# Kernel optimization log

Hardware: AMD Instinct MI355X
Metric: run time of the kernel (lower is better)

## Reference

```python
import jax, jax.numpy as jnp
import numpy as np

B, T, V = 128, 128, 30000
DE, DP, PV = 300, 30, 50
H = 300
HEADS = 6
LA, LL = 5, 24
POL = 3
RED = 10
NEG = -1e9


def entmax15(x):
    # exact 1.5-entmax along last axis (sorting algorithm, Peters & Martins 2019)
    d = x.shape[-1]
    x = x / 2.0
    x = x - jnp.max(x, axis=-1, keepdims=True)
    xs = -jnp.sort(-x, axis=-1)                      # descending
    rho = jnp.arange(1, d + 1, dtype=x.dtype)
    mean = jnp.cumsum(xs, axis=-1) / rho
    meansq = jnp.cumsum(xs * xs, axis=-1) / rho
    ss = rho * (meansq - mean * mean)
    delta = (1.0 - ss) / rho
    tau = mean - jnp.sqrt(jnp.maximum(delta, 0.0))
    support = jnp.sum((tau <= xs).astype(jnp.int32), axis=-1, keepdims=True)
    tau_star = jnp.take_along_axis(tau, support - 1, axis=-1)
    return jnp.square(jnp.maximum(x - tau_star, 0.0))


def lstm_dir(x, mask, Wih, Whh, bih, bhh, reverse):
    # packed-sequence-equivalent LSTM: state frozen / output zeroed at padded steps
    b = x.shape[0]
    h0 = jnp.zeros((b, Whh.shape[1]), x.dtype)

    def step(carry, inp):
        h, c = carry
        xt, mt = inp
        g = xt @ Wih.T + h @ Whh.T + (bih + bhh)
        i, f, gg, o = jnp.split(g, 4, axis=-1)       # torch gate order i,f,g,o
        c_new = jax.nn.sigmoid(f) * c + jax.nn.sigmoid(i) * jnp.tanh(gg)
        h_new = jax.nn.sigmoid(o) * jnp.tanh(c_new)
        m = mt[:, None]
        return (jnp.where(m, h_new, h), jnp.where(m, c_new, c)), jnp.where(m, h_new, 0.0)

    _, outs = jax.lax.scan(step, (h0, h0),
                           (jnp.swapaxes(x, 0, 1), jnp.swapaxes(mask, 0, 1)),
                           reverse=reverse)
    return jnp.swapaxes(outs, 0, 1)


def se_layer(x, valid, w1, b1, w2, b2):
    # SELayer over the SEQUENCE dim (channel == max_len); x: [b,t,d], valid: [b,t]
    y = jnp.mean(x, axis=-1)                         # adaptive avg-pool over (1, d)
    y = jax.nn.relu(y @ w1.T + b1) @ w2.T + b2
    y = y + jnp.where(valid > 0, 0.0, NEG)           # mask_2
    y = jax.nn.softmax(y, axis=1)
    return x * y[..., None]


def gcn(x, A, W, b):
    # D @ A @ D @ x @ W + b with D = diag((rowsum(A)+1)^-0.5)
    dn = (jnp.sum(A, axis=2) + 1.0) ** -0.5
    An = dn[:, :, None] * A * dn[:, None, :]
    return jnp.einsum('bij,bjd->bid', An, x) @ W + b


def _forward(text_indices, aspect_indices, left_indices, pos_indices, asp_post, height,
             adj, embed_matrix, pos_emb_w, Wih_f, Whh_f, bih_f, bhh_f,
             Wih_b, Whh_b, bih_b, bhh_b, wq, bq, wk, bk,
             se_w1, se_b1, se_w2, se_b2, gc1_w, gc1_b, gc2_w, gc2_b,
             affine1, affine2, fc_w, fc_b):
    b, t = text_indices.shape
    nonpad = text_indices != 0
    valid = nonpad.astype(jnp.float32)               # mask_ squeezed -> [b,t]
    text_len = jnp.sum(nonpad, axis=-1)
    aspect_real_len = jnp.sum(aspect_indices != 0, axis=-1)
    left_len = jnp.sum(left_indices != 0, axis=-1)   # aspect_double_idx = [left_len,left_len]

    # embedding; overwrite aspect position with mean aspect embedding
    text = embed_matrix[text_indices]
    am = (aspect_indices != 0).astype(jnp.float32)[..., None]
    asp_mean = jnp.sum(embed_matrix[aspect_indices] * am, axis=1) / aspect_real_len[:, None].astype(jnp.float32)
    text = text.at[jnp.arange(b), asp_post].set(asp_mean)
    embs = jnp.concatenate([text, pos_emb_w[pos_indices]], axis=-1)

    lenmask = jnp.arange(t)[None, :] < text_len[:, None]
    text_out = jnp.concatenate([
        lstm_dir(embs, lenmask, Wih_f, Whh_f, bih_f, bhh_f, False),
        lstm_dir(embs, lenmask, Wih_b, Whh_b, bih_b, bhh_b, True)], axis=-1)  # [b,t,2H]

    # multi-head entmax attention -> semantic adjacency
    dk = (2 * H) // HEADS
    q = (text_out @ wq.T + bq).reshape(b, t, HEADS, dk).transpose(0, 2, 1, 3)
    k = (text_out @ wk.T + bk).reshape(b, t, HEADS, dk).transpose(0, 2, 1, 3)
    scores = jnp.einsum('bhqd,bhkd->bhqk', q, k) / (dk ** 0.5)
    scores = jnp.where(nonpad[:, None, None, :], scores, NEG)
    adj_sem = jnp.mean(entmax15(scores), axis=1)     # average over heads
    eye = jnp.eye(t, dtype=adj_sem.dtype)
    adj_sem = adj_sem * (1.0 - eye) + eye            # zero diagonal, add identity
    adj_sem = valid[:, :, None] * adj_sem

    se = lambda z: se_layer(z, valid, se_w1, se_b1, se_w2, se_b2)
    # (the first x = relu(gc1(..,adj)); x = relu(gc2(..,adj)) branch is dead code:
    #  x is overwritten before use, so only the x_sem path matters)
    x_sem = jax.nn.relu(gcn(se(text_out), adj_sem, gc1_w, gc1_b))
    x = jax.nn.relu(gcn(se(x_sem), adj, gc2_w, gc2_b))

    A1 = jax.nn.softmax(jnp.einsum('bid,bjd->bij', x @ affine1, x_sem), axis=-1)
    A2 = jax.nn.softmax(jnp.einsum('bid,bjd->bij', x_sem @ affine2, x), axis=-1)
    out = jnp.concatenate([jnp.einsum('bij,bjd->bid', A1, x_sem),
                           jnp.einsum('bij,bjd->bid', A2, x)], axis=-1)  # [b,t,4H]
    aspmask = (jnp.arange(t)[None, :] == left_len[:, None]).astype(jnp.float32)
    pooled = jnp.sum(out * aspmask[..., None], axis=1)  # keep aspect token only
    return pooled @ fc_w + fc_b                         # [b, POL]


def setup_inputs():
    key = jax.random.key(0)
    ks = jax.random.split(key, 36)
    f32 = jnp.float32
    pos_t = jnp.arange(T)[None, :]
    text_len = jax.random.randint(ks[0], (B,), T // 2, T + 1)
    text_indices = jax.random.randint(ks[1], (B, T), 1, V) * (pos_t < text_len[:, None])
    asp_len = jax.random.randint(ks[2], (B,), 1, LA + 1)
    aspect_indices = jax.random.randint(ks[3], (B, LA), 1, V) * (jnp.arange(LA)[None, :] < asp_len[:, None])
    left_len = jax.random.randint(ks[4], (B,), 1, LL + 1)
    left_indices = jax.random.randint(ks[5], (B, LL), 1, V) * (jnp.arange(LL)[None, :] < left_len[:, None])
    pos_indices = jax.random.randint(ks[6], (B, T), 1, PV) * (pos_t < text_len[:, None])
    vmask = (pos_t < text_len[:, None]).astype(f32)
    adj = (jax.random.uniform(ks[7], (B, T, T)) < 0.08).astype(f32)
    adj = adj * vmask[:, :, None] * vmask[:, None, :]
    asp_post = left_len                              # aspect sits right after left context
    height = jax.random.randint(ks[8], (B, T + 1), 1, 12)

    def rn(k, shape, scale=0.05):
        return jax.random.normal(k, shape, dtype=f32) * scale

    params = dict(
        embed_matrix=rn(ks[9], (V, DE), 0.5),
        pos_emb_w=rn(ks[10], (PV, DP), 0.5).at[0].set(0.0),
        Wih_f=rn(ks[11], (4 * H, DE + DP)), Whh_f=rn(ks[12], (4 * H, H)),
        bih_f=rn(ks[13], (4 * H,)), bhh_f=rn(ks[14], (4 * H,)),
        Wih_b=rn(ks[15], (4 * H, DE + DP)), Whh_b=rn(ks[16], (4 * H, H)),
        bih_b=rn(ks[17], (4 * H,)), bhh_b=rn(ks[18], (4 * H,)),
        wq=rn(ks[19], (2 * H, 2 * H)), bq=rn(ks[20], (2 * H,)),
        wk=rn(ks[21], (2 * H, 2 * H)), bk=rn(ks[22], (2 * H,)),
        se_w1=rn(ks[23], (T // RED, T)), se_b1=rn(ks[24], (T // RED,)),
        se_w2=rn(ks[25], (T, T // RED)), se_b2=rn(ks[26], (T,)),
        gc1_w=rn(ks[27], (2 * H, 2 * H)), gc1_b=rn(ks[28], (2 * H,)),
        gc2_w=rn(ks[29], (2 * H, 2 * H)), gc2_b=rn(ks[30], (2 * H,)),
        affine1=rn(ks[31], (2 * H, 2 * H)), affine2=rn(ks[32], (2 * H, 2 * H)),
        fc_w=rn(ks[33], (4 * H, POL)), fc_b=rn(ks[34], (POL,)),
    )
    return dict(text_indices=text_indices, aspect_indices=aspect_indices,
                left_indices=left_indices, pos_indices=pos_indices,
                asp_post=asp_post, height=height, adj=adj, **params)


def reference(text_indices, aspect_indices, left_indices, pos_indices, asp_post, height,
              adj, embed_matrix, pos_emb_w, Wih_f, Whh_f, bih_f, bhh_f,
              Wih_b, Whh_b, bih_b, bhh_b, wq, bq, wk, bk,
              se_w1, se_b1, se_w2, se_b2, gc1_w, gc1_b, gc2_w, gc2_b,
              affine1, affine2, fc_w, fc_b):
    return _forward(text_indices, aspect_indices, left_indices, pos_indices, asp_post, height,
                    adj, embed_matrix, pos_emb_w, Wih_f, Whh_f, bih_f, bhh_f,
                    Wih_b, Whh_b, bih_b, bhh_b, wq, bq, wk, bk,
                    se_w1, se_b1, se_w2, se_b2, gc1_w, gc1_b, gc2_w, gc2_b,
                    affine1, affine2, fc_w, fc_b)
```

## Files before the change

kernel.cpp:

```cpp
#include <hip/hip_runtime.h>

typedef unsigned short ushort_t;
typedef unsigned int   uint_t;
typedef __attribute__((ext_vector_type(8))) short short8;
typedef __attribute__((ext_vector_type(4))) float floatx4;

#define NEGV -1000000000.0f

__device__ __forceinline__ float bf2f(ushort_t h){ return __uint_as_float(((uint_t)h)<<16); }
__device__ __forceinline__ ushort_t f2bf(float f){
  uint_t u = __float_as_uint(f);
  uint_t r = u + 0x7fffu + ((u>>16)&1u);
  return (ushort_t)(r>>16);
}
__device__ __forceinline__ float wredsum(float v){ for(int o=32;o;o>>=1) v += __shfl_xor(v,o); return v; }
__device__ __forceinline__ float wredmax(float v){ for(int o=32;o;o>>=1) v = fmaxf(v,__shfl_xor(v,o)); return v; }
__device__ __forceinline__ int   wredsumi(int v){ for(int o=32;o;o>>=1) v += __shfl_xor(v,o); return v; }

__device__ __forceinline__ short8 ldg_cohr(const ushort_t* p){
  short8 r;
  asm volatile("global_load_dwordx4 %0, %1, off sc0 sc1"
               : "=&v"(r) : "v"(p) : "memory");
  return r;
}
__device__ __forceinline__ void stg_b128_cohr(ushort_t* p, short8 v){
  asm volatile("global_store_dwordx4 %0, %1, off sc0 sc1" :: "v"(p), "v"(v) : "memory");
}

__device__ __forceinline__ float fsig(float x){ return 1.f/(1.f+__expf(-x)); }
__device__ __forceinline__ float ftanh(float x){ return 1.f - 2.f/(1.f+__expf(2.f*x)); }

__global__ void k_cvt8(const void* __restrict__ src, ushort_t* __restrict__ dst,
                       long n, const ushort_t* __restrict__ probe_src){
  __shared__ int sflag;
  if (threadIdx.x < 64){
    ushort_t u = probe_src[2*threadIdx.x];
    int e = (u>>7)&0xFF;
    int c = (e>=100 && e<=140) ? 1 : 0;
    c = wredsumi(c);
    if (threadIdx.x==0) sflag = (c>32) ? 1 : 0;
  }
  __syncthreads();
  bool isbf = (sflag!=0);
  long base = (blockIdx.x*256L + threadIdx.x)*8;
  if (base>=n) return;
  if (isbf){
    if (base+8<=n) *(uint4*)(dst+base) = *(const uint4*)((const ushort_t*)src+base);
    else for (long i=base;i<n;i++) dst[i]=((const ushort_t*)src)[i];
  } else {
    const float* s = (const float*)src;
    if (base+8<=n){
      float4 v0 = *(const float4*)(s+base);
      float4 v1 = *(const float4*)(s+base+4);
      ushort_t o[8] = {f2bf(v0.x),f2bf(v0.y),f2bf(v0.z),f2bf(v0.w),
                       f2bf(v1.x),f2bf(v1.y),f2bf(v1.z),f2bf(v1.w)};
      *(uint4*)(dst+base) = *(uint4*)o;
    } else {
      for (long i=base;i<n;i++) dst[i]=f2bf(s[i]);
    }
  }
}

struct CvtTab { const void* src[25]; ushort_t* dst[25]; long n[25]; };

__global__ void k_cvt8_multi(CvtTab tab, const ushort_t* __restrict__ probe_src){
  __shared__ int sflag;
  if (threadIdx.x < 64){
    ushort_t u = probe_src[2*threadIdx.x];
    int e = (u>>7)&0xFF;
    int c = (e>=100 && e<=140) ? 1 : 0;
    c = wredsumi(c);
    if (threadIdx.x==0) sflag = (c>32) ? 1 : 0;
  }
  __syncthreads();
  bool isbf = (sflag!=0);
  int ix = blockIdx.y;
  long n = tab.n[ix];
  long base = (blockIdx.x*256L + threadIdx.x)*8;
  if (base>=n) return;
  const void* src = tab.src[ix];
  ushort_t* dst = tab.dst[ix];
  if (isbf){
    if (base+8<=n) *(uint4*)(dst+base) = *(const uint4*)((const ushort_t*)src+base);
    else for (long i=base;i<n;i++) dst[i]=((const ushort_t*)src)[i];
  } else {
    const float* s = (const float*)src;
    if (base+8<=n){
      float4 v0 = *(const float4*)(s+base);
      float4 v1 = *(const float4*)(s+base+4);
      ushort_t o[8] = {f2bf(v0.x),f2bf(v0.y),f2bf(v0.z),f2bf(v0.w),
                       f2bf(v1.x),f2bf(v1.y),f2bf(v1.z),f2bf(v1.w)};
      *(uint4*)(dst+base) = *(uint4*)o;
    } else {
      for (long i=base;i<n;i++) dst[i]=f2bf(s[i]);
    }
  }
}

__device__ __forceinline__ bool probe_is_bf16(const ushort_t* probe_src){
  int c=0;
  #pragma unroll 1
  for (int i=0;i<64;i++){
    ushort_t u = probe_src[2*i];
    int e = (u>>7)&0xFF;
    c += (e>=100 && e<=140) ? 1 : 0;
  }
  return c>32;
}

__global__ void k_lens(const int* __restrict__ ti, const int* __restrict__ li,
                       int* __restrict__ nonpad, int* __restrict__ text_len,
                       int* __restrict__ left_len){
  int b = blockIdx.x, t = threadIdx.x;
  nonpad[b*128+t] = (ti[b*128+t]!=0) ? 1 : 0;
  if (t==0){
    int c=0; for (int k2=0;k2<128;k2++) c += (ti[b*128+k2]!=0);
    text_len[b]=c;
    int l=0; for (int k2=0;k2<24;k2++) l += (li[b*24+k2]!=0);
    left_len[b]=l;
  }
}

__global__ void k_aspmean(const int* __restrict__ ai, const ushort_t* __restrict__ em,
                          float* __restrict__ asp_mean){
  int b = blockIdx.x;
  int idxs[5]; int cnt=0;
  for (int a=0;a<5;a++){ int ix=ai[b*5+a]; idxs[a]=ix; cnt += (ix!=0); }
  float inv = 1.0f/(float)cnt;
  for (int d=threadIdx.x; d<300; d+=128){
    float s=0.f;
    for (int a=0;a<5;a++) if (idxs[a]) s += bf2f(em[(long)idxs[a]*300+d]);
    asp_mean[b*300+d] = s*inv;
  }
}

__global__ void k_embs(const int* __restrict__ ti, const int* __restrict__ pi,
                       const int* __restrict__ asp_post,
                       const ushort_t* __restrict__ em, const ushort_t* __restrict__ pe,
                       const float* __restrict__ asp_mean, ushort_t* __restrict__ embs){
  int blk = blockIdx.x;
  int b = blk>>7, t = blk&127;
  int ap = asp_post[b];
  int tix = ti[b*128+t];
  int pix = pi[b*128+t];
  for (int col=threadIdx.x; col<336; col+=128){
    ushort_t v;
    if (col<300) v = (t==ap) ? f2bf(asp_mean[b*300+col]) : em[(long)tix*300+col];
    else if (col<330) v = pe[pix*30 + (col-300)];
    else v = 0;
    embs[(long)(b*128+t)*336 + col] = v;
  }
}

__global__ void k_padwih2(const ushort_t* __restrict__ src, ushort_t* __restrict__ dst){
  int i = blockIdx.x*blockDim.x + threadIdx.x;
  if (i >= 1280*336) return;
  int r = i/336, k = i - r*336;
  int j = r>>2, gate = r&3;
  ushort_t v = 0;
  if (j<300 && k<330) v = src[(long)(gate*300+j)*330 + k];
  dst[i] = v;
}

__global__ void k_padwhh2(const ushort_t* __restrict__ src, ushort_t* __restrict__ dst){
  int i = blockIdx.x*blockDim.x + threadIdx.x;
  if (i >= 1280*320) return;
  int r = i/320, k = i - r*320;
  int j = r>>2, gate = r&3;
  ushort_t v = 0;
  if (j<300 && k<300) v = src[(long)(gate*300+j)*300 + k];
  dst[i] = v;
}

__global__ void k_biassum2(const ushort_t* __restrict__ a, const ushort_t* __restrict__ b,
                           float* __restrict__ dst){
  int i = blockIdx.x*blockDim.x + threadIdx.x;
  if (i>=1280) return;
  int j = i>>2, g = i&3;
  dst[i] = (j<300) ? (bf2f(a[g*300+j]) + bf2f(b[g*300+j])) : 0.f;
}

__global__ void k_biascvt(const ushort_t* __restrict__ a, float* __restrict__ dst, int n){
  int i = blockIdx.x*blockDim.x + threadIdx.x;
  if (i<n) dst[i] = bf2f(a[i]);
}

__global__ void k_padzero(ushort_t* __restrict__ qh, ushort_t* __restrict__ kh){
  int i = blockIdx.x*blockDim.x + threadIdx.x;
  if (i >= 98304*4*2) return;
  int half = (i >= 98304*4) ? 1 : 0;
  int j = i - half*98304*4;
  int row = j>>2, c = 100 + (j&3);
  (half ? kh : qh)[(long)row*104 + c] = 0;
}

template<int TB, int MODE>
__global__ __launch_bounds__(256) void gemm_k(
    int M, int N, int K,
    const ushort_t* __restrict__ A, long lda, long sAz,
    const ushort_t* __restrict__ B, long ldb, long sBz,
    float* __restrict__ Cf, ushort_t* __restrict__ Cb, long ldc, long sCz,
    const float* __restrict__ bias, int relu,
    const float* __restrict__ rowscale,
    const int* __restrict__ nonpad)
{
  __shared__ ushort_t As[128*40];
  __shared__ ushort_t Bs[128*40];
  const int tid = threadIdx.x;
  const int m0 = blockIdx.x*128, n0 = blockIdx.y*128;
  const int z = blockIdx.z;
  const ushort_t* Ap = A + (long)z*sAz;
  const ushort_t* Bp = B + (long)z*sBz;
  floatx4 acc[4][4];
  #pragma unroll
  for (int i=0;i<4;i++)
    #pragma unroll
    for (int j=0;j<4;j++){ acc[i][j][0]=0.f; acc[i][j][1]=0.f; acc[i][j][2]=0.f; acc[i][j][3]=0.f; }
  const int w = tid>>6, wm = w&1, wn = w>>1;
  const int lane = tid&63, lr = lane&15, lq = lane>>4;

  for (int k0=0;k0<K;k0+=32){
    #pragma unroll
    for (int c2=0;c2<2;c2++){
      int ch = tid + 256*c2;
      int row = ch>>2, kc = (ch&3)*8;
      int gr = m0+row, gk = k0+kc;
      uint4 v{};
      if (gr<M && gk<K) v = *(const uint4*)(Ap + (long)gr*lda + gk);
      *(uint4*)(&As[row*40+kc]) = v;
    }
    if (TB){
      #pragma unroll
      for (int c2=0;c2<2;c2++){
        int ch = tid + 256*c2;
        int row = ch>>2, kc = (ch&3)*8;
        int gn = n0+row, gk = k0+kc;
        uint4 v{};
        if (gn<N && gk<K) v = *(const uint4*)(Bp + (long)gn*ldb + gk);
        int sw = kc ^ (((row>>3)&3)<<3);
        *(uint4*)(&Bs[row*40+sw]) = v;
      }
    } else {
      #pragma unroll
      for (int c2=0;c2<2;c2++){
        int ch = tid + 256*c2;
        int kk = ch>>4, nc = (ch&15)*8;
        int gk = k0+kk, gn = n0+nc;
        uint4 v{};
        if (gk<K && gn<N) v = *(const uint4*)(Bp + (long)gk*ldb + gn);
        uint_t wsv[4] = {v.x, v.y, v.z, v.w};
        #pragma unroll
        for (int e=0;e<8;e++){
          ushort_t hv = (e&1) ? (ushort_t)(wsv[e>>1]>>16) : (ushort_t)(wsv[e>>1]&0xffffu);
          int n = nc+e;
          int sw = kk ^ (((n>>3)&3)<<3);
          Bs[n*40+sw] = hv;
        }
      }
    }
    __syncthreads();
    short8 af[4], bfv[4];
    #pragma unroll
    for (int i=0;i<4;i++) af[i] = *(const short8*)(&As[(wm*64+i*16+lr)*40 + lq*8]);
    #pragma unroll
    for (int j=0;j<4;j++){
      int n = wn*64+j*16+lr;
      int sw = (lq*8) ^ (((n>>3)&3)<<3);
      bfv[j] = *(const short8*)(&Bs[n*40+sw]);
    }
    #pragma unroll
    for (int i=0;i<4;i++)
      #pragma unroll
      for (int j=0;j<4;j++)
        acc[i][j] = __builtin_amdgcn_mfma_f32_16x16x32_bf16(af[i], bfv[j], acc[i][j], 0,0,0);
    __syncthreads();
  }

  #pragma unroll
  for (int i=0;i<4;i++){
    #pragma unroll
    for (int j=0;j<4;j++){
      #pragma unroll
      for (int r=0;r<4;r++){
        int row = m0 + wm*64 + i*16 + lq*4 + r;
        int col = n0 + wn*64 + j*16 + lr;
        if (row<M && col<N){
          float v = acc[i][j][r];
          if (rowscale) v *= rowscale[(long)z*M + row];
          if (bias) v += bias[col];
          if (relu && v<0.f) v = 0.f;
          if (MODE==1){
            Cb[(long)z*sCz + (long)row*ldc + col] = f2bf(v);
          } else if (MODE==2){
            int b = row>>7, t = row&127;
            int h = col/100, d = col - h*100;
            Cb[ ((long)((b*6+h)*128+t))*104 + d ] = f2bf(v);
          } else if (MODE==3){
            v *= 0.1f;
            if (!nonpad[(z/6)*128 + col]) v = NEGV;
            Cf[(long)z*sCz + (long)row*ldc + col] = v;
          }
        }
      }
    }
  }
}

#define BLD 328
#define HXD 40

__global__ __launch_bounds__(512,1) void lstm2_k(
    const ushort_t* __restrict__ whh2f, const ushort_t* __restrict__ whh2b,
    const ushort_t* __restrict__ gipf, const ushort_t* __restrict__ gipb,
    ushort_t* __restrict__ hbuf,
    int* __restrict__ barr,
    ushort_t* __restrict__ text_out, const int* __restrict__ text_len,
    ushort_t* __restrict__ dumpb)
{
  __shared__ ushort_t Blds[64*BLD];
  __shared__ ushort_t hx[64*HXD];

  const int bx = blockIdx.x;
  const int slice = bx % 10;
  const int grp   = bx / 10;
  const int dir = grp & 1, bh = grp >> 1;
  const ushort_t* __restrict__ whh = dir ? whh2b : whh2f;
  const ushort_t* __restrict__ gip = dir ? gipb : gipf;
  ushort_t* hb = hbuf + (long)dir * (2L*128*320);
  int* flg = barr + grp*160;

  const int tid = threadIdx.x;
  const int w = tid>>6, lane = tid&63, lr = lane&15, lq = lane>>4;
  const int wm = w&3, wn = w>>2;

  short8 a[2][10];
  #pragma unroll
  for (int mi=0;mi<2;mi++){
    const ushort_t* ar = whh + (long)(slice*128 + (wm*2+mi)*16 + lr)*320 + lq*8;
    #pragma unroll
    for (int kf=0;kf<10;kf++) a[mi][kf] = *(const short8*)(ar + kf*32);
  }
  #pragma unroll
  for (int mi=0;mi<2;mi++)
    #pragma unroll
    for (int kf=0;kf<10;kf++)
      asm volatile("" : "+v"(a[mi][kf]));

  int jj_[2], b_[2], bl_[2], tl_[2];
  #pragma unroll
  for (int mi=0;mi<2;mi++) jj_[mi] = slice*32 + wm*8 + mi*4 + lq;
  #pragma unroll
  for (int ni=0;ni<2;ni++){
    bl_[ni] = wn*32 + ni*16 + lr;
    b_[ni]  = bh*64 + bl_[ni];
    tl_[ni] = text_len[b_[ni]];
  }

  const int boff0 = (wn*32+   lr)*BLD + lq*8;
  const int boff1 = (wn*32+16+lr)*BLD + lq*8;

  float    c_st[2][2];
  ushort_t h_st[2][2];
  #pragma unroll
  for (int mi=0;mi<2;mi++){ c_st[mi][0]=0.f; c_st[mi][1]=0.f; h_st[mi][0]=0; h_st[mi][1]=0; }

  uint2 gp[2][2];
  {
    int t0 = dir ? 127 : 0;
    #pragma unroll
    for (int mi=0;mi<2;mi++)
      #pragma unroll
      for (int ni=0;ni<2;ni++)
        gp[mi][ni] = *(const uint2*)(gip + ((long)(b_[ni]*128 + t0))*1280 + jj_[mi]*4);
  }

  for (int s=0; s<128; s++){
    const int t = dir ? (127-s) : s;
    const ushort_t* rb = hb + (long)(s&1)*(128L*320);
    ushort_t*       wb = hb + (long)((s+1)&1)*(128L*320);

    short8 tmp[5]; int ro_[5], ch_[5];
    #pragma unroll
    for (int k=0;k<5;k++){
      int c = tid + k*512;
      int row = c/40, ch = c - row*40;
      ro_[k]=row; ch_[k]=ch;
      tmp[k] = ldg_cohr(rb + (long)(bh*64+row)*320 + ch*8);
    }
    asm volatile("s_waitcnt vmcnt(0)" ::: "memory");
    __builtin_amdgcn_sched_barrier(0);
    #pragma unroll
    for (int k=0;k<5;k++)
      *(short8*)(&Blds[ro_[k]*BLD + ch_[k]*8]) = tmp[k];
    __syncthreads();

    floatx4 acc[2][2];
    #pragma unroll
    for (int mi=0;mi<2;mi++)
      #pragma unroll
      for (int ni=0;ni<2;ni++){ acc[mi][ni][0]=0.f; acc[mi][ni][1]=0.f; acc[mi][ni][2]=0.f; acc[mi][ni][3]=0.f; }
    #pragma unroll
    for (int kf=0;kf<10;kf++){
      short8 b0 = *(const short8*)(&Blds[boff0 + kf*32]);
      short8 b1 = *(const short8*)(&Blds[boff1 + kf*32]);
      acc[0][0] = __builtin_amdgcn_mfma_f32_16x16x32_bf16(a[0][kf], b0, acc[0][0], 0,0,0);
      acc[0][1] = __builtin_amdgcn_mfma_f32_16x16x32_bf16(a[0][kf], b1, acc[0][1], 0,0,0);
      acc[1][0] = __builtin_amdgcn_mfma_f32_16x16x32_bf16(a[1][kf], b0, acc[1][0], 0,0,0);
      acc[1][1] = __builtin_amdgcn_mfma_f32_16x16x32_bf16(a[1][kf], b1, acc[1][1], 0,0,0);
    }

    ushort_t tov[2][2];
    #pragma unroll
    for (int mi=0;mi<2;mi++){
      #pragma unroll
      for (int ni=0;ni<2;ni++){
        float g_i = acc[mi][ni][0] + bf2f((ushort_t)(gp[mi][ni].x & 0xffffu));
        float g_f = acc[mi][ni][1] + bf2f((ushort_t)(gp[mi][ni].x >> 16));
        float g_g = acc[mi][ni][2] + bf2f((ushort_t)(gp[mi][ni].y & 0xffffu));
        float g_o = acc[mi][ni][3] + bf2f((ushort_t)(gp[mi][ni].y >> 16));
        float ig = fsig(g_i);
        float fg = fsig(g_f);
        float gg = ftanh(g_g);
        float og = fsig(g_o);
        float cn = fg*c_st[mi][ni] + ig*gg;
        float hn = og*ftanh(cn);
        bool m = (t < tl_[ni]);
        if (m) c_st[mi][ni] = cn;
        ushort_t hv = m ? f2bf(hn) : h_st[mi][ni];
        h_st[mi][ni] = hv;
        hx[bl_[ni]*HXD + wm*8 + mi*4 + lq] = hv;
        tov[mi][ni] = m ? f2bf(hn) : (ushort_t)0;
      }
    }
    __syncthreads();

    if (tid < 256){
      int row = tid>>2, jj8 = (tid&3)*8;
      short8 hvv = *(const short8*)(&hx[row*HXD + jj8]);
      stg_b128_cohr(wb + (long)(bh*64+row)*320 + slice*32 + jj8, hvv);
    }
    #pragma unroll
    for (int mi=0;mi<2;mi++)
      #pragma unroll
      for (int ni=0;ni<2;ni++){
        ushort_t* toa = (jj_[mi] < 300)
          ? &text_out[((long)(b_[ni]*128 + t))*600 + dir*300 + jj_[mi]]
          : &dumpb[tid*4 + mi*2 + ni];
        *toa = tov[mi][ni];
      }
    {
      int tn = dir ? ((s<127) ? (126-s) : 127) : ((s<127) ? (s+1) : 0);
      #pragma unroll
      for (int mi=0;mi<2;mi++)
        #pragma unroll
        for (int ni=0;ni<2;ni++)
          gp[mi][ni] = *(const uint2*)(gip + ((long)(b_[ni]*128 + tn))*1280 + jj_[mi]*4);
    }
    asm volatile("s_waitcnt vmcnt(8)" ::: "memory");
    __syncthreads();

    if (tid==0)
      __hip_atomic_store(&flg[slice*16], s+1, __ATOMIC_RELAXED, __HIP_MEMORY_SCOPE_AGENT);
    {
      bool done = false;
      do {
        int f = 0x7fffffff;
        if (lane < 10)
          f = __hip_atomic_load(&flg[lane*16], __ATOMIC_RELAXED, __HIP_MEMORY_SCOPE_AGENT);
        done = (bool)__all(f >= s+1);
        if (!done) __builtin_amdgcn_s_sleep(1);
      } while(!done);
    }
  }
}

__global__ __launch_bounds__(64) void k_entmax(float* __restrict__ p){
  long row = blockIdx.x;
  float* base = p + row*128;
  __shared__ float xo[128], xs[128], c1[128], c2[128];
  int t = threadIdx.x;
  float a = base[t]*0.5f, b = base[t+64]*0.5f;
  float m = wredmax(fmaxf(a,b));
  a -= m; b -= m;
  xo[t]=a; xo[t+64]=b; xs[t]=a; xs[t+64]=b;
  __syncthreads();
  for (int k2=2;k2<=128;k2<<=1){
    for (int j=k2>>1;j>0;j>>=1){
      int i = ((t & ~(j-1))<<1) | (t & (j-1));
      int ixj = i | j;
      float vi = xs[i], vj = xs[ixj];
      bool blk = (i & k2)==0;
      bool sw = blk ? (vi < vj) : (vi > vj);
      __syncthreads();
      if (sw){ xs[i]=vj; xs[ixj]=vi; }
      __syncthreads();
    }
  }
  c1[t]=xs[t];       c2[t]=xs[t]*xs[t];
  c1[t+64]=xs[t+64]; c2[t+64]=xs[t+64]*xs[t+64];
  __syncthreads();
  for (int d=1; d<128; d<<=1){
    float a1 = (t>=d)     ? c1[t-d]    : 0.f;
    float a2 = (t>=d)     ? c2[t-d]    : 0.f;
    float b1 = (t+64>=d)  ? c1[t+64-d] : 0.f;
    float b2 = (t+64>=d)  ? c2[t+64-d] : 0.f;
    float x1=c1[t], y1=c2[t], x2=c1[t+64], y2=c2[t+64];
    __syncthreads();
    c1[t]=x1+a1; c2[t]=y1+a2; c1[t+64]=x2+b1; c2[t+64]=y2+b2;
    __syncthreads();
  }
  float tau_a, tau_b; int cnt=0;
  {
    float rho = (float)(t+1);
    float mean = c1[t]/rho, msq = c2[t]/rho;
    float ss = rho*(msq-mean*mean);
    float delta = (1.f-ss)/rho;
    tau_a = mean - sqrtf(fmaxf(delta,0.f));
    cnt += (tau_a <= xs[t]) ? 1 : 0;
  }
  {
    float rho = (float)(t+65);
    float mean = c1[t+64]/rho, msq = c2[t+64]/rho;
    float ss = rho*(msq-mean*mean);
    float delta = (1.f-ss)/rho;
    tau_b = mean - sqrtf(fmaxf(delta,0.f));
    cnt += (tau_b <= xs[t+64]) ? 1 : 0;
  }
  __syncthreads();
  c1[t]=tau_a; c1[t+64]=tau_b;
  __syncthreads();
  int support = wredsumi(cnt);
  support = (support<1) ? 1 : ((support>128) ? 128 : support);
  float tau_star = c1[support-1];
  float oa = fmaxf(xo[t]-tau_star, 0.f);
  float ob = fmaxf(xo[t+64]-tau_star, 0.f);
  base[t] = oa*oa; base[t+64] = ob*ob;
}

__global__ void k_adjsem(const float* __restrict__ p, const int* __restrict__ nonpad,
                         ushort_t* __restrict__ adj_sem){
  int idx = blockIdx.x*blockDim.x + threadIdx.x;
  if (idx >= 128*128*128) return;
  int b = idx>>14, rem = idx&16383, i = rem>>7, j = rem&127;
  float s = 0.f;
  for (int h=0;h<6;h++) s += p[(long)b*98304 + h*16384 + i*128 + j];
  float v = s/6.0f;
  if (i==j) v = 1.0f;
  if (!nonpad[b*128+i]) v = 0.f;
  adj_sem[idx] = f2bf(v);
}

__global__ __launch_bounds__(64) void k_dn(const ushort_t* __restrict__ src, float* __restrict__ dnv){
  long row = blockIdx.x;
  int l = threadIdx.x;
  float s = bf2f(src[row*128+l]) + bf2f(src[row*128+l+64]);
  s = wredsum(s);
  if (l==0) dnv[row] = 1.0f/sqrtf(s+1.0f);
}

__global__ __launch_bounds__(64) void k_mean(const ushort_t* __restrict__ X, float* __restrict__ ymean){
  long row = blockIdx.x;
  float s=0.f;
  for (int d=threadIdx.x; d<600; d+=64) s += bf2f(X[row*600+d]);
  s = wredsum(s);
  if (threadIdx.x==0) ymean[row] = s/600.0f;
}

__global__ void k_senet(const float* __restrict__ ymean,
                        const ushort_t* __restrict__ w1, const ushort_t* __restrict__ b1,
                        const ushort_t* __restrict__ w2, const ushort_t* __restrict__ b2,
                        const int* __restrict__ nonpad, float* __restrict__ ysoft){
  int b = blockIdx.x, t = threadIdx.x;
  __shared__ float yv[128], z1[12], red[128];
  yv[t] = ymean[b*128+t];
  __syncthreads();
  if (t<12){
    float s = bf2f(b1[t]);
    for (int k2=0;k2<128;k2++) s += yv[k2]*bf2f(w1[t*128+k2]);
    z1[t] = fmaxf(s,0.f);
  }
  __syncthreads();
  float v = bf2f(b2[t]);
  for (int r=0;r<12;r++) v += z1[r]*bf2f(w2[t*12+r]);
  if (!nonpad[b*128+t]) v += NEGV;
  red[t]=v; __syncthreads();
  for (int s2=64;s2>0;s2>>=1){ if (t<s2) red[t]=fmaxf(red[t],red[t+s2]); __syncthreads(); }
  float mx = red[0]; __syncthreads();
  float e = expf(v-mx);
  red[t]=e; __syncthreads();
  for (int s2=64;s2>0;s2>>=1){ if (t<s2) red[t]+=red[t+s2]; __syncthreads(); }
  float sm = red[0];
  ysoft[b*128+t] = e/sm;
}

__global__ void k_scale2(const ushort_t* __restrict__ X, const float* __restrict__ ysoft,
                         const float* __restrict__ dnv, ushort_t* __restrict__ out){
  int i = blockIdx.x*blockDim.x + threadIdx.x;
  if (i >= 128*128*600) return;
  int row = i/600;
  out[i] = f2bf(bf2f(X[i])*ysoft[row]*dnv[row]);
}

__global__ void k_gather(const ushort_t* __restrict__ X, const int* __restrict__ left_len,
                         ushort_t* __restrict__ dst){
  int b = blockIdx.x;
  int lb = left_len[b];
  for (int d=threadIdx.x; d<600; d+=128)
    dst[b*600+d] = X[(long)(b*128+lb)*600+d];
}

__global__ __launch_bounds__(256) void k_pool(const ushort_t* __restrict__ g,
                                              const ushort_t* __restrict__ X,
                                              float* __restrict__ pooled, int poff){
  int b = blockIdx.x, tid = threadIdx.x;
  __shared__ float gs[600], sbuf[128], red[256];
  for (int d=tid; d<600; d+=256) gs[d] = bf2f(g[b*600+d]);
  __syncthreads();
  int wv = tid>>6, lane = tid&63;
  for (int jj=wv; jj<128; jj+=4){
    float s=0.f;
    for (int d=lane; d<600; d+=64) s += gs[d]*bf2f(X[(long)(b*128+jj)*600+d]);
    s = wredsum(s);
    if (lane==0) sbuf[jj]=s;
  }
  __syncthreads();
  float v = (tid<128) ? sbuf[tid] : -3.4e38f;
  red[tid]=v; __syncthreads();
  for (int s2=128;s2>0;s2>>=1){ if (tid<s2) red[tid]=fmaxf(red[tid],red[tid+s2]); __syncthreads(); }
  float mx = red[0]; __syncthreads();
  float e = (tid<128) ? expf(v-mx) : 0.f;
  red[tid]=e; __syncthreads();
  for (int s2=128;s2>0;s2>>=1){ if (tid<s2) red[tid]+=red[tid+s2]; __syncthreads(); }
  float sm = red[0]; __syncthreads();
  if (tid<128) sbuf[tid] = e/sm;
  __syncthreads();
  for (int d=tid; d<600; d+=256){
    float acc=0.f;
    for (int j=0;j<128;j++) acc += sbuf[j]*bf2f(X[(long)(b*128+j)*600+d]);
    pooled[(long)b*1200 + poff + d] = acc;
  }
}

__global__ __launch_bounds__(64) void k_final(const float* __restrict__ pooled,
                                              const ushort_t* __restrict__ fcw,
                                              const ushort_t* __restrict__ fcb,
                                              void* __restrict__ out,
                                              const ushort_t* __restrict__ probe_src){
  bool isbf = probe_is_bf16(probe_src);
  int b = blockIdx.x, lane = threadIdx.x;
  for (int p=0;p<3;p++){
    float s=0.f;
    for (int d=lane; d<1200; d+=64) s += pooled[(long)b*1200+d]*bf2f(fcw[d*3+p]);
    s = wredsum(s);
    if (lane==0){
      float r = s + bf2f(fcb[p]);
      if (isbf) ((ushort_t*)out)[b*3+p] = f2bf(r);
      else      ((float*)out)[b*3+p] = r;
    }
  }
}

extern "C" void kernel_launch(void* const* d_in, const int* in_sizes, int n_in,
                              void* d_out, int out_size, void* d_ws, size_t ws_size,
                              hipStream_t stream) {
  const int*      ti   = (const int*)d_in[0];
  const int*      ai   = (const int*)d_in[1];
  const int*      li   = (const int*)d_in[2];
  const int*      pi   = (const int*)d_in[3];
  const int*      aps  = (const int*)d_in[4];
  const ushort_t* probe = (const ushort_t*)d_in[7];

  char* w = (char*)d_ws; size_t off = 0;
  auto alloc = [&](size_t bytes)->char*{ char* p = w+off; off = (off+bytes+255)&~(size_t)255; return p; };

  int*   text_len = (int*)alloc(512);
  int*   left_len = (int*)alloc(512);
  int*   nonpad   = (int*)alloc(65536);
  float* asp_mean = (float*)alloc(153600);
  float* dn1      = (float*)alloc(65536);
  float* dn2      = (float*)alloc(65536);
  float* ymean    = (float*)alloc(65536);
  float* ysoft    = (float*)alloc(65536);
  ushort_t* wihpf = (ushort_t*)alloc(860160);
  ushort_t* wihpb = (ushort_t*)alloc(860160);
  ushort_t* whh2f = (ushort_t*)alloc(819200);
  ushort_t* whh2b = (ushort_t*)alloc(819200);
  ushort_t* hbuf  = (ushort_t*)alloc(327680);
  int*      barr  = (int*)alloc(4096);
  ushort_t* dumpb = (ushort_t*)alloc(4096);
  float* biasgf   = (float*)alloc(5120);
  float* biasgb   = (float*)alloc(5120);
  float* bqf      = (float*)alloc(2400);
  float* bkf      = (float*)alloc(2400);
  float* gc1bf    = (float*)alloc(2400);
  float* gc2bf    = (float*)alloc(2400);
  ushort_t* g1    = (ushort_t*)alloc(153600);
  ushort_t* g2    = (ushort_t*)alloc(153600);
  ushort_t* xr    = (ushort_t*)alloc(153600);
  ushort_t* xsr   = (ushort_t*)alloc(153600);
  float* pooled   = (float*)alloc(614400);
  ushort_t* adj_c  = (ushort_t*)alloc(4194304);
  ushort_t* pe_c   = (ushort_t*)alloc(2048);
  ushort_t* wihf_c = (ushort_t*)alloc(792000);
  ushort_t* wihb_c = (ushort_t*)alloc(792000);
  ushort_t* whhf_c = (ushort_t*)alloc(720000);
  ushort_t* whhb_c = (ushort_t*)alloc(720000);
  ushort_t* bihf_c = (ushort_t*)alloc(2400);
  ushort_t* bhhf_c = (ushort_t*)alloc(2400);
  ushort_t* bihb_c = (ushort_t*)alloc(2400);
  ushort_t* bhhb_c = (ushort_t*)alloc(2400);
  ushort_t* wq_c   = (ushort_t*)alloc(720000);
  ushort_t* bq_c   = (ushort_t*)alloc(1200);
  ushort_t* wk_c   = (ushort_t*)alloc(720000);
  ushort_t* bk_c   = (ushort_t*)alloc(1200);
  ushort_t* sw1_c  = (ushort_t*)alloc(3072);
  ushort_t* sb1_c  = (ushort_t*)alloc(256);
  ushort_t* sw2_c  = (ushort_t*)alloc(3072);
  ushort_t* sb2_c  = (ushort_t*)alloc(256);
  ushort_t* g1w_c  = (ushort_t*)alloc(720000);
  ushort_t* g1b_c  = (ushort_t*)alloc(1200);
  ushort_t* g2w_c  = (ushort_t*)alloc(720000);
  ushort_t* g2b_c  = (ushort_t*)alloc(1200);
  ushort_t* af1_c  = (ushort_t*)alloc(720000);
  ushort_t* af2_c  = (ushort_t*)alloc(720000);
  ushort_t* fcw_c  = (ushort_t*)alloc(7200);
  ushort_t* fcb_c  = (ushort_t*)alloc(256);
  ushort_t* embs  = (ushort_t*)alloc(11010048);
  ushort_t* textout = (ushort_t*)alloc(19660800);
  char* R = alloc(95420416);
  ushort_t* em_c    = (ushort_t*)(R);
  ushort_t* gip_f   = (ushort_t*)(R);
  ushort_t* gip_b   = (ushort_t*)(R+41943040);
  ushort_t* qh      = (ushort_t*)(R);
  ushort_t* kh      = (ushort_t*)(R+20447232);
  float*    scores  = (float*)(R+40894464);
  ushort_t* adj_sem = (ushort_t*)(R+91226112);
  ushort_t* se_x    = (ushort_t*)(R+40894464);
  ushort_t* Zb      = (ushort_t*)(R+60555264);
  ushort_t* x_sem   = (ushort_t*)(R);
  ushort_t* xb      = (ushort_t*)(R+20447232);
  (void)ws_size; (void)n_in; (void)in_sizes; (void)out_size;

  k_cvt8<<<(9000000/8+255)/256,256,0,stream>>>(d_in[7], em_c, 9000000L, probe);
  k_cvt8<<<(2097152/8+255)/256,256,0,stream>>>(d_in[6], adj_c, 2097152L, probe);
  {
    CvtTab tab;
    const int idx[25] = {8,9,13,10,14,11,12,15,16,17,18,19,20,21,22,23,24,25,26,27,28,29,30,31,32};
    ushort_t* dl[25] = {pe_c,wihf_c,wihb_c,whhf_c,whhb_c,bihf_c,bhhf_c,bihb_c,bhhb_c,
                        wq_c,bq_c,wk_c,bk_c,sw1_c,sb1_c,sw2_c,sb2_c,
                        g1w_c,g1b_c,g2w_c,g2b_c,af1_c,af2_c,fcw_c,fcb_c};
    const long nl[25] = {900,396000,396000,360000,360000,1200,1200,1200,1200,
                         360000,600,360000,600,1536,12,1536,128,
                         360000,600,360000,600,360000,360000,3600,3};
    for (int i=0;i<25;i++){ tab.src[i]=d_in[idx[i]]; tab.dst[i]=dl[i]; tab.n[i]=nl[i]; }
    k_cvt8_multi<<<dim3(194,25),256,0,stream>>>(tab, probe);
  }

  k_lens<<<128,128,0,stream>>>(ti, li, nonpad, text_len, left_len);
  k_aspmean<<<128,128,0,stream>>>(ai, em_c, asp_mean);
  k_embs<<<16384,128,0,stream>>>(ti, pi, aps, em_c, pe_c, asp_mean, embs);
  k_padwih2<<<(1280*336+255)/256,256,0,stream>>>(wihf_c, wihpf);
  k_padwih2<<<(1280*336+255)/256,256,0,stream>>>(wihb_c, wihpb);
  k_padwhh2<<<(1280*320+255)/256,256,0,stream>>>(whhf_c, whh2f);
  k_padwhh2<<<(1280*320+255)/256,256,0,stream>>>(whhb_c, whh2b);
  k_biassum2<<<(1280+255)/256,256,0,stream>>>(bihf_c, bhhf_c, biasgf);
  k_biassum2<<<(1280+255)/256,256,0,stream>>>(bihb_c, bhhb_c, biasgb);
  k_biascvt<<<3,256,0,stream>>>(bq_c, bqf, 600);
  k_biascvt<<<3,256,0,stream>>>(bk_c, bkf, 600);
  k_biascvt<<<3,256,0,stream>>>(g1b_c, gc1bf, 600);
  k_biascvt<<<3,256,0,stream>>>(g2b_c, gc2bf, 600);

  gemm_k<1,1><<<dim3(128,10,1),256,0,stream>>>(16384,1280,336, embs,336,0, wihpf,336,0,
        nullptr, gip_f,1280,0, biasgf,0,nullptr,nullptr);
  gemm_k<1,1><<<dim3(128,10,1),256,0,stream>>>(16384,1280,336, embs,336,0, wihpb,336,0,
        nullptr, gip_b,1280,0, biasgb,0,nullptr,nullptr);

  hipMemsetAsync(hbuf, 0, 327680, stream);
  hipMemsetAsync(barr, 0, 4096, stream);
  lstm2_k<<<40,512,0,stream>>>(whh2f, whh2b, gip_f, gip_b, hbuf, barr, textout, text_len, dumpb);

  k_padzero<<<(98304*4*2+255)/256,256,0,stream>>>(qh, kh);
  gemm_k<1,2><<<dim3(128,5,1),256,0,stream>>>(16384,600,600, textout,600,0, wq_c,600,0,
        nullptr, qh,0,0, bqf,0,nullptr,nullptr);
  gemm_k<1,2><<<dim3(128,5,1),256,0,stream>>>(16384,600,600, textout,600,0, wk_c,600,0,
        nullptr, kh,0,0, bkf,0,nullptr,nullptr);

  gemm_k<1,3><<<dim3(1,1,768),256,0,stream>>>(128,128,104, qh,104,13312, kh,104,13312,
        scores, nullptr, 128, 16384, nullptr,0,nullptr, nonpad);

  k_entmax<<<98304,64,0,stream>>>(scores);

  k_adjsem<<<(2097152+255)/256,256,0,stream>>>(scores, nonpad, adj_sem);
  k_dn<<<16384,64,0,stream>>>(adj_sem, dn1);
  k_dn<<<16384,64,0,stream>>>(adj_c, dn2);

  k_mean<<<16384,64,0,stream>>>(textout, ymean);
  k_senet<<<128,128,0,stream>>>(ymean, sw1_c,sb1_c,sw2_c,sb2_c, nonpad, ysoft);
  k_scale2<<<(9830400+255)/256,256,0,stream>>>(textout, ysoft, dn1, se_x);
  gemm_k<0,1><<<dim3(1,5,128),256,0,stream>>>(128,600,128, adj_sem,128,16384, se_x,600,76800,
        nullptr, Zb,600,76800, nullptr,0, dn1, nullptr);
  gemm_k<0,1><<<dim3(128,5,1),256,0,stream>>>(16384,600,600, Zb,600,0, g1w_c,600,0,
        nullptr, x_sem,600,0, gc1bf,1,nullptr,nullptr);

  k_mean<<<16384,64,0,stream>>>(x_sem, ymean);
  k_senet<<<128,128,0,stream>>>(ymean, sw1_c,sb1_c,sw2_c,sb2_c, nonpad, ysoft);
  k_scale2<<<(9830400+255)/256,256,0,stream>>>(x_sem, ysoft, dn2, se_x);
  gemm_k<0,1><<<dim3(1,5,128),256,0,stream>>>(128,600,128, adj_c,128,16384, se_x,600,76800,
        nullptr, Zb,600,76800, nullptr,0, dn2, nullptr);
  gemm_k<0,1><<<dim3(128,5,1),256,0,stream>>>(16384,600,600, Zb,600,0, g2w_c,600,0,
        nullptr, xb,600,0, gc2bf,1,nullptr,nullptr);

  k_gather<<<128,128,0,stream>>>(xb, left_len, xr);
  k_gather<<<128,128,0,stream>>>(x_sem, left_len, xsr);
  gemm_k<0,1><<<dim3(1,5,1),256,0,stream>>>(128,600,600, xr,600,0, af1_c,600,0,
        nullptr, g1,600,0, nullptr,0,nullptr,nullptr);
  gemm_k<0,1><<<dim3(1,5,1),256,0,stream>>>(128,600,600, xsr,600,0, af2_c,600,0,
        nullptr, g2,600,0, nullptr,0,nullptr,nullptr);
  k_pool<<<128,256,0,stream>>>(g1, x_sem, pooled, 0);
  k_pool<<<128,256,0,stream>>>(g2, xb, pooled, 600);

  k_final<<<128,64,0,stream>>>(pooled, fcw_c, fcb_c, d_out, probe);
}
```

Measured before the change: 1.793 ms.

## Replace cross-block barrier LSTM with per-block batch-group LSTM using LDS hidden state

The recurrent LSTM kernel no longer splits the hidden dimension across 10 cooperating blocks that sync through global-memory flags and coherent global h buffers. Instead each of 16 blocks (1024 threads) owns 16 sequences of one direction, keeps h double-buffered in LDS, and uses only __syncthreads per step. This removes the grid-wide spin barrier and global h round trips. In exchange only 16 CUs are used, and W_hh is re-streamed from global/L2 every step instead of staying in registers, with a non-unrolled k loop.

```diff
diff --git a/kernel.cpp b/kernel.cpp
--- a/kernel.cpp
+++ b/kernel.cpp
@@ -16,16 +16,6 @@
 __device__ __forceinline__ float wredsum(float v){ for(int o=32;o;o>>=1) v += __shfl_xor(v,o); return v; }
 __device__ __forceinline__ float wredmax(float v){ for(int o=32;o;o>>=1) v = fmaxf(v,__shfl_xor(v,o)); return v; }
 __device__ __forceinline__ int   wredsumi(int v){ for(int o=32;o;o>>=1) v += __shfl_xor(v,o); return v; }
-
-__device__ __forceinline__ short8 ldg_cohr(const ushort_t* p){
-  short8 r;
-  asm volatile("global_load_dwordx4 %0, %1, off sc0 sc1"
-               : "=&v"(r) : "v"(p) : "memory");
-  return r;
-}
-__device__ __forceinline__ void stg_b128_cohr(ushort_t* p, short8 v){
-  asm volatile("global_store_dwordx4 %0, %1, off sc0 sc1" :: "v"(p), "v"(v) : "memory");
-}
 
 __device__ __forceinline__ float fsig(float x){ return 1.f/(1.f+__expf(-x)); }
 __device__ __forceinline__ float ftanh(float x){ return 1.f - 2.f/(1.f+__expf(2.f*x)); }
@@ -306,171 +296,96 @@
   }
 }
 
-#define BLD 328
-#define HXD 40
-
-__global__ __launch_bounds__(512,1) void lstm2_k(
+#define HLD 328
+
+__global__ __launch_bounds__(1024,1) void lstm3_k(
     const ushort_t* __restrict__ whh2f, const ushort_t* __restrict__ whh2b,
     const ushort_t* __restrict__ gipf, const ushort_t* __restrict__ gipb,
-    ushort_t* __restrict__ hbuf,
-    int* __restrict__ barr,
-    ushort_t* __restrict__ text_out, const int* __restrict__ text_len,
-    ushort_t* __restrict__ dumpb)
+    ushort_t* __restrict__ text_out, const int* __restrict__ text_len)
 {
-  __shared__ ushort_t Blds[64*BLD];
-  __shared__ ushort_t hx[64*HXD];
+  __shared__ ushort_t hbufs[2][16*HLD];
 
   const int bx = blockIdx.x;
-  const int slice = bx % 10;
-  const int grp   = bx / 10;
-  const int dir = grp & 1, bh = grp >> 1;
+  const int dir = bx & 1, bg = bx >> 1;
   const ushort_t* __restrict__ whh = dir ? whh2b : whh2f;
   const ushort_t* __restrict__ gip = dir ? gipb : gipf;
-  ushort_t* hb = hbuf + (long)dir * (2L*128*320);
-  int* flg = barr + grp*160;
 
   const int tid = threadIdx.x;
   const int w = tid>>6, lane = tid&63, lr = lane&15, lq = lane>>4;
-  const int wm = w&3, wn = w>>2;
-
-  short8 a[2][10];
+
+  for (int i=tid; i<2*16*HLD; i+=1024) ((ushort_t*)hbufs)[i] = 0;
+
+  int jj_[5];
   #pragma unroll
-  for (int mi=0;mi<2;mi++){
-    const ushort_t* ar = whh + (long)(slice*128 + (wm*2+mi)*16 + lr)*320 + lq*8;
-    #pragma unroll
-    for (int kf=0;kf<10;kf++) a[mi][kf] = *(const short8*)(ar + kf*32);
-  }
+  for (int mi=0;mi<5;mi++) jj_[mi] = w*20 + mi*4 + lq;
+  const int b  = bg*16 + lr;
+  const int tl = text_len[b];
+  const long gibase = (long)b*128;
+
+  float    c_st[5];
+  ushort_t h_st[5];
   #pragma unroll
-  for (int mi=0;mi<2;mi++)
-    #pragma unroll
-    for (int kf=0;kf<10;kf++)
-      asm volatile("" : "+v"(a[mi][kf]));
-
-  int jj_[2], b_[2], bl_[2], tl_[2];
-  #pragma unroll
-  for (int mi=0;mi<2;mi++) jj_[mi] = slice*32 + wm*8 + mi*4 + lq;
-  #pragma unroll
-  for (int ni=0;ni<2;ni++){
-    bl_[ni] = wn*32 + ni*16 + lr;
-    b_[ni]  = bh*64 + bl_[ni];
-    tl_[ni] = text_len[b_[ni]];
-  }
-
-  const int boff0 = (wn*32+   lr)*BLD + lq*8;
-  const int boff1 = (wn*32+16+lr)*BLD + lq*8;
-
-  float    c_st[2][2];
-  ushort_t h_st[2][2];
-  #pragma unroll
-  for (int mi=0;mi<2;mi++){ c_st[mi][0]=0.f; c_st[mi][1]=0.f; h_st[mi][0]=0; h_st[mi][1]=0; }
-
-  uint2 gp[2][2];
-  {
-    int t0 = dir ? 127 : 0;
-    #pragma unroll
-    for (int mi=0;mi<2;mi++)
-      #pragma unroll
-      for (int ni=0;ni<2;ni++)
-        gp[mi][ni] = *(const uint2*)(gip + ((long)(b_[ni]*128 + t0))*1280 + jj_[mi]*4);
-  }
-
+  for (int mi=0;mi<5;mi++){ c_st[mi]=0.f; h_st[mi]=0; }
+
+  const ushort_t* abase = whh + (long)(w*80 + lr)*320 + lq*8;
+
+  __syncthreads();
+
+  #pragma unroll 1
   for (int s=0; s<128; s++){
     const int t = dir ? (127-s) : s;
-    const ushort_t* rb = hb + (long)(s&1)*(128L*320);
-    ushort_t*       wb = hb + (long)((s+1)&1)*(128L*320);
-
-    short8 tmp[5]; int ro_[5], ch_[5];
-    #pragma unroll
-    for (int k=0;k<5;k++){
-      int c = tid + k*512;
-      int row = c/40, ch = c - row*40;
-      ro_[k]=row; ch_[k]=ch;
-      tmp[k] = ldg_cohr(rb + (long)(bh*64+row)*320 + ch*8);
-    }
-    asm volatile("s_waitcnt vmcnt(0)" ::: "memory");
-    __builtin_amdgcn_sched_barrier(0);
-    #pragma unroll
-    for (int k=0;k<5;k++)
-      *(short8*)(&Blds[ro_[k]*BLD + ch_[k]*8]) = tmp[k];
+    const ushort_t* hb = hbufs[s&1];
+    ushort_t*       hw = hbufs[(s+1)&1];
+
+    uint2 gp[5];
+    #pragma unroll
+    for (int mi=0;mi<5;mi++)
+      gp[mi] = *(const uint2*)(gip + (gibase + t)*1280 + jj_[mi]*4);
+
+    floatx4 acc[5];
+    #pragma unroll
+    for (int mi=0;mi<5;mi++){ acc[mi][0]=0.f; acc[mi][1]=0.f; acc[mi][2]=0.f; acc[mi][3]=0.f; }
+
+    short8 a0[5], a1[5];
+    #pragma unroll
+    for (int mi=0;mi<5;mi++) a0[mi] = *(const short8*)(abase + (long)mi*16*320);
+    #pragma unroll 1
+    for (int kf=0; kf<10; kf++){
+      if (kf<9){
+        #pragma unroll
+        for (int mi=0;mi<5;mi++)
+          a1[mi] = *(const short8*)(abase + (long)mi*16*320 + (kf+1)*32);
+      }
+      short8 bf = *(const short8*)(&hb[lr*HLD + kf*32 + lq*8]);
+      #pragma unroll
+      for (int mi=0;mi<5;mi++)
+        acc[mi] = __builtin_amdgcn_mfma_f32_16x16x32_bf16(a0[mi], bf, acc[mi], 0,0,0);
+      #pragma unroll
+      for (int mi=0;mi<5;mi++) a0[mi] = a1[mi];
+    }
+
+    #pragma unroll
+    for (int mi=0;mi<5;mi++){
+      float g_i = acc[mi][0] + bf2f((ushort_t)(gp[mi].x & 0xffffu));
+      float g_f = acc[mi][1] + bf2f((ushort_t)(gp[mi].x >> 16));
+      float g_g = acc[mi][2] + bf2f((ushort_t)(gp[mi].y & 0xffffu));
+      float g_o = acc[mi][3] + bf2f((ushort_t)(gp[mi].y >> 16));
+      float ig = fsig(g_i);
+      float fg = fsig(g_f);
+      float gg = ftanh(g_g);
+      float og = fsig(g_o);
+      float cn = fg*c_st[mi] + ig*gg;
+      float hv_f = og*ftanh(cn);
+      bool m = (t < tl);
+      if (m) c_st[mi] = cn;
+      ushort_t hv = m ? f2bf(hv_f) : h_st[mi];
+      h_st[mi] = hv;
+      if (jj_[mi] < 300){
+        hw[lr*HLD + jj_[mi]] = hv;
+        text_out[(gibase + t)*600 + dir*300 + jj_[mi]] = m ? f2bf(hv_f) : (ushort_t)0;
+      }
+    }
     __syncthreads();
-
-    floatx4 acc[2][2];
-    #pragma unroll
-    for (int mi=0;mi<2;mi++)
-      #pragma unroll
-      for (int ni=0;ni<2;ni++){ acc[mi][ni][0]=0.f; acc[mi][ni][1]=0.f; acc[mi][ni][2]=0.f; acc[mi][ni][3]=0.f; }
-    #pragma unroll
-    for (int kf=0;kf<10;kf++){
-      short8 b0 = *(const short8*)(&Blds[boff0 + kf*32]);
-      short8 b1 = *(const short8*)(&Blds[boff1 + kf*32]);
-      acc[0][0] = __builtin_amdgcn_mfma_f32_16x16x32_bf16(a[0][kf], b0, acc[0][0], 0,0,0);
-      acc[0][1] = __builtin_amdgcn_mfma_f32_16x16x32_bf16(a[0][kf], b1, acc[0][1], 0,0,0);
-      acc[1][0] = __builtin_amdgcn_mfma_f32_16x16x32_bf16(a[1][kf], b0, acc[1][0], 0,0,0);
-      acc[1][1] = __builtin_amdgcn_mfma_f32_16x16x32_bf16(a[1][kf], b1, acc[1][1], 0,0,0);
-    }
-
-    ushort_t tov[2][2];
-    #pragma unroll
-    for (int mi=0;mi<2;mi++){
-      #pragma unroll
-      for (int ni=0;ni<2;ni++){
-        float g_i = acc[mi][ni][0] + bf2f((ushort_t)(gp[mi][ni].x & 0xffffu));
-        float g_f = acc[mi][ni][1] + bf2f((ushort_t)(gp[mi][ni].x >> 16));
-        float g_g = acc[mi][ni][2] + bf2f((ushort_t)(gp[mi][ni].y & 0xffffu));
-        float g_o = acc[mi][ni][3] + bf2f((ushort_t)(gp[mi][ni].y >> 16));
-        float ig = fsig(g_i);
-        float fg = fsig(g_f);
-        float gg = ftanh(g_g);
-        float og = fsig(g_o);
-        float cn = fg*c_st[mi][ni] + ig*gg;
-        float hn = og*ftanh(cn);
-        bool m = (t < tl_[ni]);
-        if (m) c_st[mi][ni] = cn;
-        ushort_t hv = m ? f2bf(hn) : h_st[mi][ni];
-        h_st[mi][ni] = hv;
-        hx[bl_[ni]*HXD + wm*8 + mi*4 + lq] = hv;
-        tov[mi][ni] = m ? f2bf(hn) : (ushort_t)0;
-      }
-    }
-    __syncthreads();
-
-    if (tid < 256){
-      int row = tid>>2, jj8 = (tid&3)*8;
-      short8 hvv = *(const short8*)(&hx[row*HXD + jj8]);
-      stg_b128_cohr(wb + (long)(bh*64+row)*320 + slice*32 + jj8, hvv);
-    }
-    #pragma unroll
-    for (int mi=0;mi<2;mi++)
-      #pragma unroll
-      for (int ni=0;ni<2;ni++){
-        ushort_t* toa = (jj_[mi] < 300)
-          ? &text_out[((long)(b_[ni]*128 + t))*600 + dir*300 + jj_[mi]]
-          : &dumpb[tid*4 + mi*2 + ni];
-        *toa = tov[mi][ni];
-      }
-    {
-      int tn = dir ? ((s<127) ? (126-s) : 127) : ((s<127) ? (s+1) : 0);
-      #pragma unroll
-      for (int mi=0;mi<2;mi++)
-        #pragma unroll
-        for (int ni=0;ni<2;ni++)
-          gp[mi][ni] = *(const uint2*)(gip + ((long)(b_[ni]*128 + tn))*1280 + jj_[mi]*4);
-    }
-    asm volatile("s_waitcnt vmcnt(8)" ::: "memory");
-    __syncthreads();
-
-    if (tid==0)
-      __hip_atomic_store(&flg[slice*16], s+1, __ATOMIC_RELAXED, __HIP_MEMORY_SCOPE_AGENT);
-    {
-      bool done = false;
-      do {
-        int f = 0x7fffffff;
-        if (lane < 10)
-          f = __hip_atomic_load(&flg[lane*16], __ATOMIC_RELAXED, __HIP_MEMORY_SCOPE_AGENT);
-        done = (bool)__all(f >= s+1);
-        if (!done) __builtin_amdgcn_s_sleep(1);
-      } while(!done);
-    }
   }
 }
 
@@ -685,9 +600,6 @@
   ushort_t* wihpb = (ushort_t*)alloc(860160);
   ushort_t* whh2f = (ushort_t*)alloc(819200);
   ushort_t* whh2b = (ushort_t*)alloc(819200);
-  ushort_t* hbuf  = (ushort_t*)alloc(327680);
-  int*      barr  = (int*)alloc(4096);
-  ushort_t* dumpb = (ushort_t*)alloc(4096);
   float* biasgf   = (float*)alloc(5120);
   float* biasgb   = (float*)alloc(5120);
   float* bqf      = (float*)alloc(2400);
@@ -775,9 +687,7 @@
   gemm_k<1,1><<<dim3(128,10,1),256,0,stream>>>(16384,1280,336, embs,336,0, wihpb,336,0,
         nullptr, gip_b,1280,0, biasgb,0,nullptr,nullptr);
 
-  hipMemsetAsync(hbuf, 0, 327680, stream);
-  hipMemsetAsync(barr, 0, 4096, stream);
-  lstm2_k<<<40,512,0,stream>>>(whh2f, whh2b, gip_f, gip_b, hbuf, barr, textout, text_len, dumpb);
+  lstm3_k<<<16,1024,0,stream>>>(whh2f, whh2b, gip_f, gip_b, textout, text_len);
 
   k_padzero<<<(98304*4*2+255)/256,256,0,stream>>>(qh, kh);
   gemm_k<1,2><<<dim3(128,5,1),256,0,stream>>>(16384,600,600, textout,600,0, wq_c,600,0,
```

After: 4.121 ms. 2.3x slower.
